# Performance work log

Measured on AMD Instinct MI355X. Metric: run time of the kernel, lower is better.

## Reference

```python
import jax, jax.numpy as jnp
import numpy as np

B, N, E, H, EXP = 16, 1024, 768, 8, 2
D = E // H
HID = EXP * E
SCALE = 1.0 / (E ** 0.5)  # module divides by e**0.5, not d_head**0.5
EPS = 1e-5


def layer_norm(x, g, b):
    m = jnp.mean(x, axis=-1, keepdims=True)
    v = jnp.var(x, axis=-1, keepdims=True)
    return (x - m) * jax.lax.rsqrt(v + EPS) * g + b


def setup_inputs() -> dict:
    key = jax.random.key(0)
    ks = jax.random.split(key, 8)
    s = lambda fan_in: 1.0 / np.sqrt(fan_in)
    return {
        "x": jax.random.normal(ks[0], (B, N, E), jnp.float32),
        "ln1_g": jnp.ones((E,), jnp.float32),
        "ln1_b": jnp.zeros((E,), jnp.float32),
        "qkv_w": jax.random.normal(ks[1], (E, 3 * E), jnp.float32) * s(E),
        "qkv_b": jnp.zeros((3 * E,), jnp.float32),
        "proj_w": jax.random.normal(ks[2], (E, E), jnp.float32) * s(E),
        "proj_b": jnp.zeros((E,), jnp.float32),
        "ln2_g": jnp.ones((E,), jnp.float32),
        "ln2_b": jnp.zeros((E,), jnp.float32),
        "ff1_w": jax.random.normal(ks[3], (E, HID), jnp.float32) * s(E),
        "ff1_b": jnp.zeros((HID,), jnp.float32),
        "ff2_w": jax.random.normal(ks[4], (HID, E), jnp.float32) * s(HID),
        "ff2_b": jnp.zeros((E,), jnp.float32),
    }


def reference(x, ln1_g, ln1_b, qkv_w, qkv_b, proj_w, proj_b,
              ln2_g, ln2_b, ff1_w, ff1_b, ff2_w, ff2_b):
    b, n, e = x.shape
    # --- attention sub-block (pre-norm, residual) ---
    h = layer_norm(x, ln1_g, ln1_b)
    qkv = h @ qkv_w + qkv_b                       # [b, n, 3e]
    # einops 'b n (h d t) -> t b h n d'
    qkv = qkv.reshape(b, n, H, D, 3)
    q = jnp.transpose(qkv[..., 0], (0, 2, 1, 3))   # [b, h, n, d]
    k = jnp.transpose(qkv[..., 1], (0, 2, 1, 3))
    v = jnp.transpose(qkv[..., 2], (0, 2, 1, 3))
    att = jax.nn.softmax(jnp.einsum('bhnd,bhmd->bhnm', q, k) * SCALE, axis=-1)
    out = jnp.einsum('bhnm,bhmd->bhnd', att, v)    # [b, h, n, d]
    out = jnp.transpose(out, (0, 2, 1, 3)).reshape(b, n, e)
    x = x + (out @ proj_w + proj_b)
    # --- FFN sub-block (pre-norm, residual) ---
    h = layer_norm(x, ln2_g, ln2_b)
    h = jax.nn.gelu(h @ ff1_w + ff1_b, approximate=False)
    x = x + (h @ ff2_w + ff2_b)
    return x
```

## Files before the change

kernel.cpp:

```cpp
#include <hip/hip_runtime.h>
#include <cstddef>

#define B_   16
#define N_   1024
#define E_   768
#define H_   8
#define D_   96
#define HID_ 1536
#define ROWS (B_ * N_)
#define SCALE_ 0.03608439182435161f

typedef __attribute__((ext_vector_type(8))) short bf16x8;
typedef __attribute__((ext_vector_type(4))) float f32x4;

__device__ __forceinline__ unsigned short f2bf(float f) {
    union { float f; unsigned int u; } c; c.f = f;
    unsigned int u = c.u + 0x7FFFu + ((c.u >> 16) & 1u);
    return (unsigned short)(u >> 16);
}

__device__ __forceinline__ void gload16(const void* g, void* l) {
    __builtin_amdgcn_global_load_lds(
        (const __attribute__((address_space(1))) unsigned int*)g,
        (__attribute__((address_space(3))) unsigned int*)l, 16, 0, 0);
}

__device__ __forceinline__ float gelu_exact(float x) {
    return 0.5f * x * (1.0f + erff(x * 0.7071067811865475f));
}

__global__ __launch_bounds__(256) void wcvt_kernel(const float* __restrict__ W,
                                                   unsigned short* __restrict__ Wt,
                                                   int K, int N) {
    __shared__ float t[32][33];
    int n0 = blockIdx.x * 32, k0 = blockIdx.y * 32;
    int tr = threadIdx.x >> 3;
    int tc = (threadIdx.x & 7) * 4;
    float4 v = *(const float4*)&W[(size_t)(k0 + tr) * N + n0 + tc];
    t[tr][tc + 0] = v.x; t[tr][tc + 1] = v.y; t[tr][tc + 2] = v.z; t[tr][tc + 3] = v.w;
    __syncthreads();
    ushort4 o;
    o.x = f2bf(t[tc + 0][tr]);
    o.y = f2bf(t[tc + 1][tr]);
    o.z = f2bf(t[tc + 2][tr]);
    o.w = f2bf(t[tc + 3][tr]);
    *(ushort4*)&Wt[(size_t)(n0 + tr) * K + k0 + tc] = o;
}

__global__ __launch_bounds__(256) void ln_fused_kernel(const float* __restrict__ x,
                                                       const float* __restrict__ g,
                                                       const float* __restrict__ beta,
                                                       unsigned short* __restrict__ out) {
    int row = blockIdx.x;
    int tid = threadIdx.x;
    const float* xr = x + (size_t)row * E_;
    float v0 = xr[tid];
    float v1 = xr[tid + 256];
    float v2 = xr[tid + 512];
    float s  = v0 + v1 + v2;
    float s2 = v0 * v0 + v1 * v1 + v2 * v2;
#pragma unroll
    for (int off = 32; off > 0; off >>= 1) {
        s  += __shfl_down(s, off);
        s2 += __shfl_down(s2, off);
    }
    __shared__ float sb[8];
    __shared__ float stats[2];
    int lane = tid & 63, wid = tid >> 6;
    if (lane == 0) { sb[wid] = s; sb[4 + wid] = s2; }
    __syncthreads();
    if (tid == 0) {
        float S  = sb[0] + sb[1] + sb[2] + sb[3];
        float S2 = sb[4] + sb[5] + sb[6] + sb[7];
        float m = S * (1.0f / E_);
        float var = S2 * (1.0f / E_) - m * m;
        stats[0] = m;
        stats[1] = rsqrtf(var + 1e-5f);
    }
    __syncthreads();
    float mean = stats[0], rstd = stats[1];
    unsigned short* orow = out + (size_t)row * E_;
    orow[tid]       = f2bf((v0 - mean) * rstd * g[tid]       + beta[tid]);
    orow[tid + 256] = f2bf((v1 - mean) * rstd * g[tid + 256] + beta[tid + 256]);
    orow[tid + 512] = f2bf((v2 - mean) * rstd * g[tid + 512] + beta[tid + 512]);
}

template<int MODE>
__global__ __launch_bounds__(256) void bgemm_kernel(
    const unsigned short* __restrict__ A, const unsigned short* __restrict__ Wt,
    const float* __restrict__ bias,
    const float* R, float* C, unsigned short* Cb,
    unsigned short* qo, unsigned short* ko, unsigned short* vo,
    int M, int N, int K)
{
    __shared__ __align__(16) unsigned short As[128 * 32];
    __shared__ __align__(16) unsigned short Bs[128 * 32];
    const int tid = threadIdx.x;
    const int l = tid & 63, w = tid >> 6;
    const int bm = blockIdx.y * 128, bn = blockIdx.x * 128;
    const int wr = (w >> 1) * 64, wc = (w & 1) * 64;
    const int l15 = l & 15, l4 = l >> 4;

    const int srow = w * 16 + (l >> 2);
    const int scol = (l & 3) * 8;
    const unsigned short* Ag = A  + (size_t)(bm + srow) * K + scol;
    const unsigned short* Wg = Wt + (size_t)(bn + srow) * K + scol;
    unsigned short* AsW = As + w * 512;
    unsigned short* BsW = Bs + w * 512;

    f32x4 acc[4][4] = {};

    for (int k0 = 0; k0 < K; k0 += 32) {
        __syncthreads();
        gload16(Ag + k0,                  AsW);
        gload16(Ag + (size_t)64 * K + k0, AsW + 2048);
        gload16(Wg + k0,                  BsW);
        gload16(Wg + (size_t)64 * K + k0, BsW + 2048);
        __syncthreads();
        bf16x8 af[4], bfr[4];
#pragma unroll
        for (int mi = 0; mi < 4; ++mi)
            af[mi] = *(const bf16x8*)&As[(wr + mi * 16 + l15) * 32 + l4 * 8];
#pragma unroll
        for (int ni = 0; ni < 4; ++ni)
            bfr[ni] = *(const bf16x8*)&Bs[(wc + ni * 16 + l15) * 32 + l4 * 8];
#pragma unroll
        for (int mi = 0; mi < 4; ++mi)
#pragma unroll
            for (int ni = 0; ni < 4; ++ni)
                acc[mi][ni] = __builtin_amdgcn_mfma_f32_16x16x32_bf16(
                    af[mi], bfr[ni], acc[mi][ni], 0, 0, 0);
    }

    const int r0 = bm + wr + l4 * 4;
    const int c0 = bn + wc + l15;
    float bv[4];
#pragma unroll
    for (int ni = 0; ni < 4; ++ni) bv[ni] = bias[c0 + ni * 16];

#pragma unroll
    for (int mi = 0; mi < 4; ++mi) {
#pragma unroll
        for (int r = 0; r < 4; ++r) {
            int row = r0 + mi * 16 + r;
            if constexpr (MODE == 0) {
                size_t base = (size_t)row * N;
#pragma unroll
                for (int ni = 0; ni < 4; ++ni) {
                    size_t idx = base + c0 + ni * 16;
                    C[idx] = acc[mi][ni][r] + bv[ni] + R[idx];
                }
            } else if constexpr (MODE == 1) {
                size_t base = (size_t)row * N;
#pragma unroll
                for (int ni = 0; ni < 4; ++ni) {
                    size_t idx = base + c0 + ni * 16;
                    Cb[idx] = f2bf(gelu_exact(acc[mi][ni][r] + bv[ni]));
                }
            } else {
                int b = row >> 10, ntok = row & (N_ - 1);
#pragma unroll
                for (int ni = 0; ni < 4; ++ni) {
                    int n = c0 + ni * 16;
                    int e = n / 3, t = n - e * 3;
                    int hh = e / D_, dd = e - hh * D_;
                    float cval = acc[mi][ni][r] + bv[ni];
                    size_t bh = (size_t)(b * H_ + hh);
                    if (t == 0)      qo[(bh * N_ + ntok) * D_ + dd] = f2bf(cval * SCALE_);
                    else if (t == 1) ko[(bh * N_ + ntok) * D_ + dd] = f2bf(cval);
                    else             vo[(bh * D_ + dd) * N_ + ntok] = f2bf(cval);
                }
            }
        }
    }
}

#define QT  64
#define KVT 64
#define KST 104
#define VST 88

__global__ __launch_bounds__(256) void fattn_kernel(
    const unsigned short* __restrict__ qg, const unsigned short* __restrict__ kg,
    const unsigned short* __restrict__ vtg, unsigned short* __restrict__ out) {
    int bh = blockIdx.y;
    int b = bh >> 3, h = bh & 7;
    int q0 = blockIdx.x * QT;
    int tid = threadIdx.x;
    int l = tid & 63, w = tid >> 6;
    int q16 = l & 15, g = l >> 4;
    int hi2 = (l >> 5) & 1;

    __shared__ __align__(16) unsigned short Qs[QT * KST];
    __shared__ __align__(16) unsigned short Ks[KVT * KST];
    __shared__ __align__(16) unsigned short Vts[D_ * VST];

    {
        int row = tid >> 2, c8 = (tid & 3) * 24;
        const uint4* src = (const uint4*)(qg + ((size_t)bh * N_ + q0 + row) * D_ + c8);
        uint4* dst = (uint4*)(Qs + row * KST + c8);
#pragma unroll
        for (int i = 0; i < 3; ++i) dst[i] = src[i];
    }
    __syncthreads();

    bf16x8 qf[3];
#pragma unroll
    for (int dc = 0; dc < 3; ++dc)
        qf[dc] = *(const bf16x8*)&Qs[(w * 16 + q16) * KST + dc * 32 + g * 8];

    float m_run = -INFINITY, l_run = 0.f;
    f32x4 oacc[6] = {};

    for (int kt = 0; kt < N_ / KVT; ++kt) {
        __syncthreads();
        {
            int row = tid >> 2, c8 = (tid & 3) * 24;
            const uint4* src = (const uint4*)(kg + ((size_t)bh * N_ + kt * KVT + row) * D_ + c8);
            uint4* dst = (uint4*)(Ks + row * KST + c8);
#pragma unroll
            for (int i = 0; i < 3; ++i) dst[i] = src[i];
        }
        {
            int c8 = (tid & 7) * 8;
#pragma unroll
            for (int p = 0; p < 3; ++p) {
                int row = (tid >> 3) + p * 32;
                *(uint4*)(Vts + row * VST + c8) =
                    *(const uint4*)(vtg + ((size_t)bh * D_ + row) * N_ + kt * KVT + c8);
            }
        }
        __syncthreads();

        f32x4 sacc[4] = {};
#pragma unroll
        for (int sub = 0; sub < 4; ++sub)
#pragma unroll
            for (int dc = 0; dc < 3; ++dc) {
                bf16x8 af = *(const bf16x8*)&Ks[(sub * 16 + q16) * KST + dc * 32 + g * 8];
                sacc[sub] = __builtin_amdgcn_mfma_f32_16x16x32_bf16(af, qf[dc], sacc[sub], 0, 0, 0);
            }

        float pmax = -INFINITY;
#pragma unroll
        for (int s = 0; s < 4; ++s)
#pragma unroll
            for (int r = 0; r < 4; ++r) pmax = fmaxf(pmax, sacc[s][r]);
        pmax = fmaxf(pmax, __shfl_xor(pmax, 16));
        pmax = fmaxf(pmax, __shfl_xor(pmax, 32));
        float m_new = fmaxf(m_run, pmax);
        float fac = __expf(m_run - m_new);
        float pe[4][4];
        float rs = 0.f;
#pragma unroll
        for (int s = 0; s < 4; ++s)
#pragma unroll
            for (int r = 0; r < 4; ++r) {
                pe[s][r] = __expf(sacc[s][r] - m_new);
                rs += pe[s][r];
            }
        rs += __shfl_xor(rs, 16);
        rs += __shfl_xor(rs, 32);
        l_run = l_run * fac + rs;
        m_run = m_new;
#pragma unroll
        for (int d = 0; d < 6; ++d)
#pragma unroll
            for (int r = 0; r < 4; ++r) oacc[d][r] *= fac;

        bf16x8 pf[2];
#pragma unroll
        for (int c = 0; c < 2; ++c)
#pragma unroll
            for (int e = 0; e < 8; ++e) {
                int gsrc = (((l >> 4) & 1) * 8 + e) >> 2;
                int src = q16 + (gsrc << 4);
                float va = __shfl(pe[c * 2][e & 3], src);
                float vb = __shfl(pe[c * 2 + 1][e & 3], src);
                pf[c][e] = (short)f2bf(hi2 ? vb : va);
            }

#pragma unroll
        for (int dsub = 0; dsub < 6; ++dsub)
#pragma unroll
            for (int c = 0; c < 2; ++c) {
                bf16x8 vf = *(const bf16x8*)&Vts[(dsub * 16 + q16) * VST + c * 32 + g * 8];
                oacc[dsub] = __builtin_amdgcn_mfma_f32_16x16x32_bf16(vf, pf[c], oacc[dsub], 0, 0, 0);
            }
    }

    float inv = 1.0f / l_run;
    int qrow = q0 + w * 16 + q16;
    size_t base = ((size_t)(b * N_ + qrow)) * E_ + h * D_;
#pragma unroll
    for (int dsub = 0; dsub < 6; ++dsub)
#pragma unroll
        for (int r = 0; r < 4; ++r)
            out[base + dsub * 16 + g * 4 + r] = f2bf(oacc[dsub][r] * inv);
}

extern "C" void kernel_launch(void* const* d_in, const int* in_sizes, int n_in,
                              void* d_out, int out_size, void* d_ws, size_t ws_size,
                              hipStream_t stream) {
    const float* x      = (const float*)d_in[0];
    const float* ln1_g  = (const float*)d_in[1];
    const float* ln1_b  = (const float*)d_in[2];
    const float* qkv_w  = (const float*)d_in[3];
    const float* qkv_b  = (const float*)d_in[4];
    const float* proj_w = (const float*)d_in[5];
    const float* proj_b = (const float*)d_in[6];
    const float* ln2_g  = (const float*)d_in[7];
    const float* ln2_b  = (const float*)d_in[8];
    const float* ff1_w  = (const float*)d_in[9];
    const float* ff1_b  = (const float*)d_in[10];
    const float* ff2_w  = (const float*)d_in[11];
    const float* ff2_b  = (const float*)d_in[12];
    float* out = (float*)d_out;
    float* ws  = (float*)d_ws;

    const size_t S = (size_t)ROWS * E_ / 2;
    unsigned short* qkv_wt = (unsigned short*)ws;
    unsigned short* proj_wt = qkv_wt + (size_t)3 * E_ * E_;
    unsigned short* ff1_wt  = proj_wt + (size_t)E_ * E_;
    unsigned short* ff2_wt  = ff1_wt + (size_t)HID_ * E_;
    float* Rb = ws + 2359296;
    unsigned short* h16   = (unsigned short*)(Rb);
    unsigned short* q16   = (unsigned short*)(Rb + S);
    unsigned short* k16   = (unsigned short*)(Rb + 2 * S);
    unsigned short* vt16  = (unsigned short*)(Rb + 3 * S);
    unsigned short* attnb = h16;
    unsigned short* h16b  = q16;
    unsigned short* ffh   = k16;
    float* x1 = out;

    wcvt_kernel<<<dim3(3 * E_ / 32, E_ / 32), 256, 0, stream>>>(qkv_w, qkv_wt, E_, 3 * E_);
    wcvt_kernel<<<dim3(E_ / 32, E_ / 32), 256, 0, stream>>>(proj_w, proj_wt, E_, E_);
    wcvt_kernel<<<dim3(HID_ / 32, E_ / 32), 256, 0, stream>>>(ff1_w, ff1_wt, E_, HID_);
    wcvt_kernel<<<dim3(E_ / 32, HID_ / 32), 256, 0, stream>>>(ff2_w, ff2_wt, HID_, E_);
    ln_fused_kernel<<<ROWS, 256, 0, stream>>>(x, ln1_g, ln1_b, h16);
    bgemm_kernel<2><<<dim3(3 * E_ / 128, ROWS / 128), 256, 0, stream>>>(
        h16, qkv_wt, qkv_b, nullptr, nullptr, nullptr, q16, k16, vt16,
        ROWS, 3 * E_, E_);
    fattn_kernel<<<dim3(N_ / QT, B_ * H_), 256, 0, stream>>>(q16, k16, vt16, attnb);
    bgemm_kernel<0><<<dim3(E_ / 128, ROWS / 128), 256, 0, stream>>>(
        attnb, proj_wt, proj_b, x, x1, nullptr, nullptr, nullptr, nullptr,
        ROWS, E_, E_);
    ln_fused_kernel<<<ROWS, 256, 0, stream>>>(x1, ln2_g, ln2_b, h16b);
    bgemm_kernel<1><<<dim3(HID_ / 128, ROWS / 128), 256, 0, stream>>>(
        h16b, ff1_wt, ff1_b, nullptr, nullptr, ffh, nullptr, nullptr, nullptr,
        ROWS, HID_, E_);
    bgemm_kernel<0><<<dim3(E_ / 128, ROWS / 128), 256, 0, stream>>>(
        ffh, ff2_wt, ff2_b, x1, out, nullptr, nullptr, nullptr, nullptr,
        ROWS, E_, HID_);
}
```

Baseline: 657.0 us.

## Rework flash attention: register prefetch, XOR swizzle, exp2 softmax, lazy rescale

The attention kernel now prefetches the next K/V tile into registers while computing the current tile. It replaces padded shared-memory strides with an XOR swizzle and adds an occupancy hint to launch bounds. Q is pre-scaled by log2(e) so the softmax can use exp2f, and rescaling of the running max is skipped when the new max exceeds the old one by no more than a threshold. P is packed into bf16 pairs before shuffling, which halves the shuffle count, and conversion uses the hardware bf16 path. These changes target memory latency, LDS footprint and VALU/shuffle overhead, at the cost of extra register pressure and some accuracy risk from the lazy rescale.

```diff
diff --git a/kernel.cpp b/kernel.cpp
--- a/kernel.cpp
+++ b/kernel.cpp
@@ -1,4 +1,5 @@
 #include <hip/hip_runtime.h>
+#include <hip/hip_bf16.h>
 #include <cstddef>
 
 #define B_   16
@@ -8,7 +9,8 @@
 #define D_   96
 #define HID_ 1536
 #define ROWS (B_ * N_)
-#define SCALE_ 0.03608439182435161f
+#define SCALE_  0.03608439182435161f
+#define QSCALE_ 0.052058774f
 
 typedef __attribute__((ext_vector_type(8))) short bf16x8;
 typedef __attribute__((ext_vector_type(4))) float f32x4;
@@ -17,6 +19,12 @@
     union { float f; unsigned int u; } c; c.f = f;
     unsigned int u = c.u + 0x7FFFu + ((c.u >> 16) & 1u);
     return (unsigned short)(u >> 16);
+}
+
+__device__ __forceinline__ unsigned short f2bf_hw(float f) {
+    union { __hip_bfloat16 h; unsigned short u; } c;
+    c.h = __float2bfloat16(f);
+    return c.u;
 }
 
 __device__ __forceinline__ void gload16(const void* g, void* l) {
@@ -166,7 +174,7 @@
                     int hh = e / D_, dd = e - hh * D_;
                     float cval = acc[mi][ni][r] + bv[ni];
                     size_t bh = (size_t)(b * H_ + hh);
-                    if (t == 0)      qo[(bh * N_ + ntok) * D_ + dd] = f2bf(cval * SCALE_);
+                    if (t == 0)      qo[(bh * N_ + ntok) * D_ + dd] = f2bf(cval * QSCALE_);
                     else if (t == 1) ko[(bh * N_ + ntok) * D_ + dd] = f2bf(cval);
                     else             vo[(bh * D_ + dd) * N_ + ntok] = f2bf(cval);
                 }
@@ -177,10 +185,9 @@
 
 #define QT  64
 #define KVT 64
-#define KST 104
-#define VST 88
-
-__global__ __launch_bounds__(256) void fattn_kernel(
+#define NT  (N_ / KVT)
+
+__global__ __launch_bounds__(256, 4) void fattn_kernel(
     const unsigned short* __restrict__ qg, const unsigned short* __restrict__ kg,
     const unsigned short* __restrict__ vtg, unsigned short* __restrict__ out) {
     int bh = blockIdx.y;
@@ -190,54 +197,71 @@
     int l = tid & 63, w = tid >> 6;
     int q16 = l & 15, g = l >> 4;
     int hi2 = (l >> 5) & 1;
-
-    __shared__ __align__(16) unsigned short Qs[QT * KST];
-    __shared__ __align__(16) unsigned short Ks[KVT * KST];
-    __shared__ __align__(16) unsigned short Vts[D_ * VST];
+    const int swz = (q16 & 7) << 3;
+
+    __shared__ __align__(16) unsigned short Qs[QT * D_];
+    __shared__ __align__(16) unsigned short Ks[KVT * D_];
+    __shared__ __align__(16) unsigned short Vts[D_ * KVT];
+
+    const int krow = tid >> 2, kc8 = (tid & 3) * 24;
+    const int vrow0 = tid >> 3, vc8 = (tid & 7) * 8;
 
     {
-        int row = tid >> 2, c8 = (tid & 3) * 24;
-        const uint4* src = (const uint4*)(qg + ((size_t)bh * N_ + q0 + row) * D_ + c8);
-        uint4* dst = (uint4*)(Qs + row * KST + c8);
-#pragma unroll
-        for (int i = 0; i < 3; ++i) dst[i] = src[i];
+        const uint4* src = (const uint4*)(qg + ((size_t)bh * N_ + q0 + krow) * D_ + kc8);
+        int sw = (krow & 7) << 3;
+#pragma unroll
+        for (int i = 0; i < 3; ++i)
+            *(uint4*)&Qs[(krow * D_ + kc8 + i * 8) ^ sw] = src[i];
     }
     __syncthreads();
 
     bf16x8 qf[3];
 #pragma unroll
     for (int dc = 0; dc < 3; ++dc)
-        qf[dc] = *(const bf16x8*)&Qs[(w * 16 + q16) * KST + dc * 32 + g * 8];
+        qf[dc] = *(const bf16x8*)&Qs[((w * 16 + q16) * D_ + dc * 32 + g * 8) ^ swz];
+
+    uint4 kreg[3], vreg[3];
+    {
+        const uint4* ks = (const uint4*)(kg + ((size_t)bh * N_ + krow) * D_ + kc8);
+#pragma unroll
+        for (int i = 0; i < 3; ++i) kreg[i] = ks[i];
+#pragma unroll
+        for (int p = 0; p < 3; ++p)
+            vreg[p] = *(const uint4*)(vtg + ((size_t)bh * D_ + vrow0 + p * 32) * N_ + vc8);
+    }
 
     float m_run = -INFINITY, l_run = 0.f;
     f32x4 oacc[6] = {};
 
-    for (int kt = 0; kt < N_ / KVT; ++kt) {
+    for (int kt = 0; kt < NT; ++kt) {
         __syncthreads();
         {
-            int row = tid >> 2, c8 = (tid & 3) * 24;
-            const uint4* src = (const uint4*)(kg + ((size_t)bh * N_ + kt * KVT + row) * D_ + c8);
-            uint4* dst = (uint4*)(Ks + row * KST + c8);
-#pragma unroll
-            for (int i = 0; i < 3; ++i) dst[i] = src[i];
-        }
-        {
-            int c8 = (tid & 7) * 8;
+            int sw = (krow & 7) << 3;
+#pragma unroll
+            for (int i = 0; i < 3; ++i)
+                *(uint4*)&Ks[(krow * D_ + kc8 + i * 8) ^ sw] = kreg[i];
 #pragma unroll
             for (int p = 0; p < 3; ++p) {
-                int row = (tid >> 3) + p * 32;
-                *(uint4*)(Vts + row * VST + c8) =
-                    *(const uint4*)(vtg + ((size_t)bh * D_ + row) * N_ + kt * KVT + c8);
+                int row = vrow0 + p * 32;
+                *(uint4*)&Vts[(row * KVT + vc8) ^ ((row & 7) << 3)] = vreg[p];
             }
         }
         __syncthreads();
+        if (kt + 1 < NT) {
+            const uint4* ks = (const uint4*)(kg + ((size_t)bh * N_ + (kt + 1) * KVT + krow) * D_ + kc8);
+#pragma unroll
+            for (int i = 0; i < 3; ++i) kreg[i] = ks[i];
+#pragma unroll
+            for (int p = 0; p < 3; ++p)
+                vreg[p] = *(const uint4*)(vtg + ((size_t)bh * D_ + vrow0 + p * 32) * N_ + (kt + 1) * KVT + vc8);
+        }
 
         f32x4 sacc[4] = {};
 #pragma unroll
         for (int sub = 0; sub < 4; ++sub)
 #pragma unroll
             for (int dc = 0; dc < 3; ++dc) {
-                bf16x8 af = *(const bf16x8*)&Ks[(sub * 16 + q16) * KST + dc * 32 + g * 8];
+                bf16x8 af = *(const bf16x8*)&Ks[((sub * 16 + q16) * D_ + dc * 32 + g * 8) ^ swz];
                 sacc[sub] = __builtin_amdgcn_mfma_f32_16x16x32_bf16(af, qf[dc], sacc[sub], 0, 0, 0);
             }
 
@@ -248,44 +272,54 @@
             for (int r = 0; r < 4; ++r) pmax = fmaxf(pmax, sacc[s][r]);
         pmax = fmaxf(pmax, __shfl_xor(pmax, 16));
         pmax = fmaxf(pmax, __shfl_xor(pmax, 32));
-        float m_new = fmaxf(m_run, pmax);
-        float fac = __expf(m_run - m_new);
+        if (!__all(pmax - m_run <= 11.0f)) {
+            float m_new = fmaxf(m_run, pmax);
+            float fac = exp2f(m_run - m_new);
+#pragma unroll
+            for (int d = 0; d < 6; ++d)
+#pragma unroll
+                for (int r = 0; r < 4; ++r) oacc[d][r] *= fac;
+            l_run *= fac;
+            m_run = m_new;
+        }
         float pe[4][4];
         float rs = 0.f;
 #pragma unroll
         for (int s = 0; s < 4; ++s)
 #pragma unroll
             for (int r = 0; r < 4; ++r) {
-                pe[s][r] = __expf(sacc[s][r] - m_new);
+                pe[s][r] = exp2f(sacc[s][r] - m_run);
                 rs += pe[s][r];
             }
         rs += __shfl_xor(rs, 16);
         rs += __shfl_xor(rs, 32);
-        l_run = l_run * fac + rs;
-        m_run = m_new;
-#pragma unroll
-        for (int d = 0; d < 6; ++d)
-#pragma unroll
-            for (int r = 0; r < 4; ++r) oacc[d][r] *= fac;
-
-        bf16x8 pf[2];
+        l_run += rs;
+
+        unsigned int pk[4][2];
+#pragma unroll
+        for (int s = 0; s < 4; ++s)
+#pragma unroll
+            for (int j = 0; j < 2; ++j)
+                pk[s][j] = (unsigned)f2bf_hw(pe[s][2 * j]) |
+                           ((unsigned)f2bf_hw(pe[s][2 * j + 1]) << 16);
+        union { unsigned int u[4]; bf16x8 v; } pfu[2];
 #pragma unroll
         for (int c = 0; c < 2; ++c)
 #pragma unroll
-            for (int e = 0; e < 8; ++e) {
-                int gsrc = (((l >> 4) & 1) * 8 + e) >> 2;
+            for (int j = 0; j < 4; ++j) {
+                int gsrc = (g & 1) * 2 + (j >> 1);
                 int src = q16 + (gsrc << 4);
-                float va = __shfl(pe[c * 2][e & 3], src);
-                float vb = __shfl(pe[c * 2 + 1][e & 3], src);
-                pf[c][e] = (short)f2bf(hi2 ? vb : va);
+                unsigned a = (unsigned)__shfl((int)pk[c * 2][j & 1], src);
+                unsigned bb = (unsigned)__shfl((int)pk[c * 2 + 1][j & 1], src);
+                pfu[c].u[j] = hi2 ? bb : a;
             }
 
 #pragma unroll
         for (int dsub = 0; dsub < 6; ++dsub)
 #pragma unroll
             for (int c = 0; c < 2; ++c) {
-                bf16x8 vf = *(const bf16x8*)&Vts[(dsub * 16 + q16) * VST + c * 32 + g * 8];
-                oacc[dsub] = __builtin_amdgcn_mfma_f32_16x16x32_bf16(vf, pf[c], oacc[dsub], 0, 0, 0);
+                bf16x8 vf = *(const bf16x8*)&Vts[((dsub * 16 + q16) * KVT + c * 32 + g * 8) ^ swz];
+                oacc[dsub] = __builtin_amdgcn_mfma_f32_16x16x32_bf16(vf, pfu[c].v, oacc[dsub], 0, 0, 0);
             }
     }
 
@@ -296,7 +330,7 @@
     for (int dsub = 0; dsub < 6; ++dsub)
 #pragma unroll
         for (int r = 0; r < 4; ++r)
-            out[base + dsub * 16 + g * 4 + r] = f2bf(oacc[dsub][r] * inv);
+            out[base + dsub * 16 + g * 4 + r] = f2bf_hw(oacc[dsub][r] * inv);
 }
 
 extern "C" void kernel_launch(void* const* d_in, const int* in_sizes, int n_in,
```

Measured after the change: 738.7 us. 12.4% more time.
